# Performance work log

Measured on AMD Instinct MI355X. Metric: run time of the kernel, lower is better.

Reference implementation:

```python
import jax, jax.numpy as jnp
import numpy as np

N_NODES = 100000
N_EDGES = 1600000
D_IN = 128
D_HID = 128
SCALE = 1.8
EPS = 1e-12


def setup_inputs() -> dict:
    key = jax.random.key(0)
    ks = jax.random.split(key, 7)
    x = jax.random.normal(ks[0], (N_NODES, D_IN), dtype=jnp.float32)
    W1 = jax.random.normal(ks[1], (D_HID, D_IN), dtype=jnp.float32) * 0.05
    b1 = jax.random.normal(ks[2], (D_HID,), dtype=jnp.float32) * 0.05
    W2 = jax.random.normal(ks[3], (D_HID, D_HID), dtype=jnp.float32) * 0.05
    b2 = jax.random.normal(ks[4], (D_HID,), dtype=jnp.float32) * 0.05
    src = jax.random.randint(ks[5], (N_EDGES,), 0, N_NODES, dtype=jnp.int64 if jax.config.jax_enable_x64 else jnp.int32)
    dst = jax.random.randint(ks[6], (N_EDGES,), 0, N_NODES, dtype=jnp.int64 if jax.config.jax_enable_x64 else jnp.int32)
    return {"x": x, "W1": W1, "b1": b1, "W2": W2, "b2": b2, "src": src, "dst": dst}


def reference(x, W1, b1, W2, b2, src, dst):
    N = x.shape[0]
    ones = jnp.ones((src.shape[0],), dtype=x.dtype)
    # GraphConv norm='both' degree normalizers (clamped to >=1 as in DGL)
    deg_out = jnp.maximum(jnp.zeros((N,), x.dtype).at[src].add(ones), 1.0)
    deg_in = jnp.maximum(jnp.zeros((N,), x.dtype).at[dst].add(ones), 1.0)
    norm_out = jax.lax.rsqrt(deg_out)[:, None]  # [N,1]
    norm_in = jax.lax.rsqrt(deg_in)[:, None]    # [N,1]

    def layer(h, W, b):
        # torch.nn.Linear: h @ W.T + b
        h = jnp.einsum('nd,kd->nk', h, W) + b
        # F.normalize(h, dim=1) * 1.8
        nrm = jnp.sqrt(jnp.sum(h * h, axis=1, keepdims=True))
        h = h / jnp.maximum(nrm, EPS) * SCALE
        # GraphConv (weight=False, bias=False, norm='both'):
        # D_out^{-1/2} -> sparse aggregate -> D_in^{-1/2}
        h = h * norm_out
        agg = jax.ops.segment_sum(h[src], dst, num_segments=N)
        return agg * norm_in

    h = layer(x, W1, b1)
    h = layer(h, W2, b2)
    return h
```

## Files before the change

kernel.cpp:

```cpp
#include <hip/hip_runtime.h>
#include <cstdint>
#include <cstddef>

#define D 128
#define NSCALE 1.8f
#define NEPS 1e-12f
#define EPB 2048
#define NBPAD 784
#define NLO 512
#define SCAP 9216
#define SRCB 23
#define SRCM 0x7FFFFF

typedef __attribute__((ext_vector_type(8))) short bf16x8;
typedef __attribute__((ext_vector_type(4))) float f32x4;

__device__ __forceinline__ ushort bf16_rtn(float f) {
    uint32_t u = __float_as_uint(f);
    u = u + 0x7FFFu + ((u >> 16) & 1u);
    return (ushort)(u >> 16);
}

__device__ __forceinline__ float blo(uint32_t u) { return __uint_as_float(u << 16); }
__device__ __forceinline__ float bhi(uint32_t u) { return __uint_as_float(u & 0xFFFF0000u); }

__global__ __launch_bounds__(256) void hist_high_kernel(const int* __restrict__ src,
                                                        const int* __restrict__ dst,
                                                        int* __restrict__ Hd,
                                                        int* __restrict__ Hs, int ne) {
    __shared__ int hd[256], hs[256];
    int t = threadIdx.x, b = blockIdx.x;
    hd[t] = 0; hs[t] = 0;
    __syncthreads();
    int base = b * EPB, end = min(ne, base + EPB);
    for (int i = base + t; i < end; i += 256) {
        atomicAdd(&hd[dst[i] >> 9], 1);
        atomicAdd(&hs[src[i] >> 9], 1);
    }
    __syncthreads();
    Hd[t * NBPAD + b] = hd[t];
    Hs[t * NBPAD + b] = hs[t];
}

__global__ __launch_bounds__(256) void scan_cols_kernel(int* __restrict__ Hd,
                                                        int* __restrict__ Hs,
                                                        int* __restrict__ total_d,
                                                        int* __restrict__ total_s, int nbk) {
    __shared__ int s[256];
    int* H = blockIdx.y ? Hs : Hd;
    int* tot = blockIdx.y ? total_s : total_d;
    int v = blockIdx.x, t = threadIdx.x;
    int base = v * NBPAD + 4 * t;
    int a0 = (4 * t + 0 < nbk) ? H[base + 0] : 0;
    int a1 = (4 * t + 1 < nbk) ? H[base + 1] : 0;
    int a2 = (4 * t + 2 < nbk) ? H[base + 2] : 0;
    int a3 = (4 * t + 3 < nbk) ? H[base + 3] : 0;
    int sum = a0 + a1 + a2 + a3;
    s[t] = sum;
    __syncthreads();
    #pragma unroll
    for (int off = 1; off < 256; off <<= 1) {
        int u = (t >= off) ? s[t - off] : 0;
        __syncthreads();
        s[t] += u;
        __syncthreads();
    }
    int excl = s[t] - sum;
    if (4 * t + 0 < nbk) H[base + 0] = excl;
    if (4 * t + 1 < nbk) H[base + 1] = excl + a0;
    if (4 * t + 2 < nbk) H[base + 2] = excl + a0 + a1;
    if (4 * t + 3 < nbk) H[base + 3] = excl + a0 + a1 + a2;
    if (t == 255) tot[v] = s[255];
}

__global__ __launch_bounds__(256) void scan_tot_kernel(const int* __restrict__ total_d,
                                                       const int* __restrict__ total_s,
                                                       int* __restrict__ Bd,
                                                       int* __restrict__ Bs, int hb) {
    __shared__ int s[256];
    const int* tot = blockIdx.x ? total_s : total_d;
    int* B = blockIdx.x ? Bs : Bd;
    int t = threadIdx.x;
    int val = (t < hb) ? tot[t] : 0;
    s[t] = val;
    __syncthreads();
    #pragma unroll
    for (int off = 1; off < 256; off <<= 1) {
        int u = (t >= off) ? s[t - off] : 0;
        __syncthreads();
        s[t] += u;
        __syncthreads();
    }
    if (t <= hb) B[t] = s[t] - val;
}

__global__ __launch_bounds__(256) void scatter_high_kernel(const int* __restrict__ src,
                                                           const int* __restrict__ dst,
                                                           const int* __restrict__ Hd,
                                                           const int* __restrict__ Hs,
                                                           const int* __restrict__ Bd,
                                                           const int* __restrict__ Bs,
                                                           uint32_t* __restrict__ spack,
                                                           ushort* __restrict__ ss_low,
                                                           int ne, int hb) {
    __shared__ int cur_d[256], cur_s[256];
    int t = threadIdx.x, b = blockIdx.x;
    if (t < hb) {
        cur_d[t] = Bd[t] + Hd[t * NBPAD + b];
        cur_s[t] = Bs[t] + Hs[t * NBPAD + b];
    }
    __syncthreads();
    int base = b * EPB, end = min(ne, base + EPB);
    for (int i = base + t; i < end; i += 256) {
        int d = dst[i], s = src[i];
        int pd = atomicAdd(&cur_d[d >> 9], 1);
        spack[pd] = ((uint32_t)(d & (NLO - 1)) << SRCB) | (uint32_t)s;
        int ps = atomicAdd(&cur_s[s >> 9], 1);
        ss_low[ps] = (ushort)(s & (NLO - 1));
    }
}

__global__ __launch_bounds__(1024) void bucket_sort_kernel(const uint32_t* __restrict__ spack,
                                                           const int* __restrict__ Bd,
                                                           int* __restrict__ offs,
                                                           int* __restrict__ cnt_dst,
                                                           float* __restrict__ norm_in,
                                                           int* __restrict__ ssrc, int N) {
    __shared__ int h[NLO], sc[NLO], cur[NLO];
    __shared__ int stage[SCAP];
    int t = threadIdx.x, v = blockIdx.x;
    int beg = Bd[v], end = Bd[v + 1];
    int m = end - beg;
    if (t < NLO) h[t] = 0;
    __syncthreads();
    for (int i = beg + t; i < end; i += 1024) atomicAdd(&h[spack[i] >> SRCB], 1);
    __syncthreads();
    int cnt = 0;
    if (t < NLO) { cnt = h[t]; sc[t] = cnt; }
    __syncthreads();
    #pragma unroll
    for (int off = 1; off < NLO; off <<= 1) {
        int u = (t >= off && t < NLO) ? sc[t - off] : 0;
        __syncthreads();
        if (t < NLO) sc[t] += u;
        __syncthreads();
    }
    int excl = (t < NLO) ? (sc[t] - cnt) : 0;
    int g = (v << 9) + t;
    if (t < NLO && g < N) {
        offs[g] = beg + excl;
        cnt_dst[g] = cnt;
        norm_in[g] = rsqrtf((float)max(cnt, 1));
    }
    if (m <= SCAP) {
        if (t < NLO) cur[t] = excl;
        __syncthreads();
        for (int i = beg + t; i < end; i += 1024) {
            uint32_t p = spack[i];
            int pos = atomicAdd(&cur[p >> SRCB], 1);
            stage[pos] = (int)(p & SRCM);
        }
        __syncthreads();
        for (int j = t; j < m; j += 1024) ssrc[beg + j] = stage[j];
    } else {
        if (t < NLO) cur[t] = beg + excl;
        __syncthreads();
        for (int i = beg + t; i < end; i += 1024) {
            uint32_t p = spack[i];
            int pos = atomicAdd(&cur[p >> SRCB], 1);
            ssrc[pos] = (int)(p & SRCM);
        }
    }
}

__global__ __launch_bounds__(1024) void bucket_hist_kernel(const ushort* __restrict__ ss_low,
                                                           const int* __restrict__ Bs,
                                                           float* __restrict__ norm_out, int N) {
    __shared__ int h[NLO];
    int t = threadIdx.x, v = blockIdx.x;
    int beg = Bs[v], end = Bs[v + 1];
    if (t < NLO) h[t] = 0;
    __syncthreads();
    for (int i = beg + t; i < end; i += 1024) atomicAdd(&h[(int)ss_low[i]], 1);
    __syncthreads();
    int g = (v << 9) + t;
    if (t < NLO && g < N) norm_out[g] = rsqrtf((float)max(h[t], 1));
}

__global__ __launch_bounds__(256) void mlp_mfma_kernel(const float* __restrict__ X,
                                                       const float* __restrict__ W,
                                                       const float* __restrict__ b,
                                                       const float* __restrict__ post,
                                                       ushort* __restrict__ Abuf, int N) {
    __shared__ ushort Wf[128 * 128];

    const int t = threadIdx.x;
    const int wave = t >> 6;
    const int lane = t & 63;
    const int q = lane >> 4;
    const int l16 = lane & 15;

    if (blockIdx.x == 0 && t < 16) {
        ((uint4*)(Abuf + (size_t)N * D))[t] = make_uint4(0u, 0u, 0u, 0u);
    }

    #pragma unroll
    for (int it = 0; it < 8; ++it) {
        int f = t + 256 * it;
        int j = f >> 8;
        int p = (f >> 6) & 3;
        int ln = f & 63;
        int n = 16 * j + (ln & 15);
        int k0 = 32 * p + 8 * (ln >> 4);
        const float* srcp = W + n * D + k0;
        float4 a0 = *(const float4*)(srcp);
        float4 a1 = *(const float4*)(srcp + 4);
        bf16x8 v;
        v[0] = (short)bf16_rtn(a0.x); v[1] = (short)bf16_rtn(a0.y);
        v[2] = (short)bf16_rtn(a0.z); v[3] = (short)bf16_rtn(a0.w);
        v[4] = (short)bf16_rtn(a1.x); v[5] = (short)bf16_rtn(a1.y);
        v[6] = (short)bf16_rtn(a1.z); v[7] = (short)bf16_rtn(a1.w);
        ((bf16x8*)Wf)[f] = v;
    }

    const int r0 = blockIdx.x * 128 + wave * 32;
    bf16x8 ahi[2][4], alo[2][4];
    #pragma unroll
    for (int rt = 0; rt < 2; ++rt) {
        int row = r0 + rt * 16 + l16;
        bool ok = (row < N);
        const float* xr = X + (size_t)(ok ? row : 0) * D;
        #pragma unroll
        for (int p = 0; p < 4; ++p) {
            int k0 = 32 * p + 8 * q;
            float4 a0 = ok ? *(const float4*)(xr + k0)     : make_float4(0, 0, 0, 0);
            float4 a1 = ok ? *(const float4*)(xr + k0 + 4) : make_float4(0, 0, 0, 0);
            float fv[8] = {a0.x, a0.y, a0.z, a0.w, a1.x, a1.y, a1.z, a1.w};
            bf16x8 h, l;
            #pragma unroll
            for (int e = 0; e < 8; ++e) {
                uint32_t u = __float_as_uint(fv[e]);
                h[e] = (short)(u >> 16);
                float hf = __uint_as_float(u & 0xFFFF0000u);
                l[e] = (short)(__float_as_uint(fv[e] - hf) >> 16);
            }
            ahi[rt][p] = h;
            alo[rt][p] = l;
        }
    }

    __syncthreads();

    f32x4 acc[2][8];
    #pragma unroll
    for (int rt = 0; rt < 2; ++rt)
        #pragma unroll
        for (int j = 0; j < 8; ++j) acc[rt][j] = (f32x4){0.f, 0.f, 0.f, 0.f};

    #pragma unroll
    for (int j = 0; j < 8; ++j) {
        #pragma unroll
        for (int p = 0; p < 4; ++p) {
            bf16x8 bb = ((bf16x8*)Wf)[(j * 4 + p) * 64 + lane];
            acc[0][j] = __builtin_amdgcn_mfma_f32_16x16x32_bf16(ahi[0][p], bb, acc[0][j], 0, 0, 0);
            acc[0][j] = __builtin_amdgcn_mfma_f32_16x16x32_bf16(alo[0][p], bb, acc[0][j], 0, 0, 0);
            acc[1][j] = __builtin_amdgcn_mfma_f32_16x16x32_bf16(ahi[1][p], bb, acc[1][j], 0, 0, 0);
            acc[1][j] = __builtin_amdgcn_mfma_f32_16x16x32_bf16(alo[1][p], bb, acc[1][j], 0, 0, 0);
        }
    }

    float bias[8];
    #pragma unroll
    for (int j = 0; j < 8; ++j) bias[j] = b[16 * j + l16];

    #pragma unroll
    for (int rt = 0; rt < 2; ++rt) {
        float ss[4] = {0.f, 0.f, 0.f, 0.f};
        #pragma unroll
        for (int j = 0; j < 8; ++j)
            #pragma unroll
            for (int r = 0; r < 4; ++r) {
                float v = acc[rt][j][r] + bias[j];
                acc[rt][j][r] = v;
                ss[r] += v * v;
            }
        #pragma unroll
        for (int m = 1; m <= 8; m <<= 1)
            #pragma unroll
            for (int r = 0; r < 4; ++r) ss[r] += __shfl_xor(ss[r], m);

        #pragma unroll
        for (int r = 0; r < 4; ++r) {
            int row = r0 + rt * 16 + 4 * q + r;
            if (row < N) {
                float f = NSCALE / fmaxf(sqrtf(ss[r]), NEPS) * post[row];
                #pragma unroll
                for (int j = 0; j < 8; ++j)
                    Abuf[(size_t)row * D + 16 * j + l16] = bf16_rtn(acc[rt][j][r] * f);
            }
        }
    }
}

__global__ __launch_bounds__(256) void agg_kernel(const ushort* __restrict__ A,
                                                  const int* __restrict__ sorted_src,
                                                  const int* __restrict__ offs,
                                                  const int* __restrict__ cnt,
                                                  const float* __restrict__ norm_in,
                                                  float* __restrict__ out, int N) {
    int wave = threadIdx.x >> 6;
    int n0 = (blockIdx.x * 4 + wave) * 2;
    if (n0 >= N) return;
    int lane = threadIdx.x & 63;
    int g = lane >> 4;
    int c = lane & 15;
    const ushort* Ac = A + c * 8;

    int n1 = n0 + 1;
    int beg0 = offs[n0], len0 = cnt[n0];
    int beg1 = 0, len1 = 0;
    if (n1 < N) { beg1 = offs[n1]; len1 = cnt[n1]; }
    int last0 = beg0 + len0 - 1;
    int last1 = beg1 + len1 - 1;

    float a0[8] = {0.f, 0.f, 0.f, 0.f, 0.f, 0.f, 0.f, 0.f};
    float a1[8] = {0.f, 0.f, 0.f, 0.f, 0.f, 0.f, 0.f, 0.f};

    int mx = max(len0, len1);
    for (int i = 0; i < mx; i += 16) {
        int idx[8];
        #pragma unroll
        for (int k = 0; k < 4; ++k) {
            int e = beg0 + i + g + 4 * k;
            int cl = max(min(e, last0), 0);
            idx[k] = sorted_src[cl];
            if (e > last0) idx[k] = N;
        }
        #pragma unroll
        for (int k = 0; k < 4; ++k) {
            int e = beg1 + i + g + 4 * k;
            int cl = max(min(e, last1), 0);
            idx[4 + k] = sorted_src[cl];
            if (e > last1) idx[4 + k] = N;
        }
        uint4 w[8];
        #pragma unroll
        for (int k = 0; k < 8; ++k) w[k] = *(const uint4*)(Ac + (size_t)idx[k] * D);
        #pragma unroll
        for (int k = 0; k < 4; ++k) {
            a0[0] += blo(w[k].x); a0[1] += bhi(w[k].x);
            a0[2] += blo(w[k].y); a0[3] += bhi(w[k].y);
            a0[4] += blo(w[k].z); a0[5] += bhi(w[k].z);
            a0[6] += blo(w[k].w); a0[7] += bhi(w[k].w);
        }
        #pragma unroll
        for (int k = 4; k < 8; ++k) {
            a1[0] += blo(w[k].x); a1[1] += bhi(w[k].x);
            a1[2] += blo(w[k].y); a1[3] += bhi(w[k].y);
            a1[4] += blo(w[k].z); a1[5] += bhi(w[k].z);
            a1[6] += blo(w[k].w); a1[7] += bhi(w[k].w);
        }
    }

    #pragma unroll
    for (int e = 0; e < 8; ++e) {
        a0[e] += __shfl_xor(a0[e], 16);
        a0[e] += __shfl_xor(a0[e], 32);
        a1[e] += __shfl_xor(a1[e], 16);
        a1[e] += __shfl_xor(a1[e], 32);
    }

    if (g == 0) {
        float sc0 = norm_in[n0];
        float* op0 = out + (size_t)n0 * D + c * 8;
        *(float4*)(op0)     = make_float4(a0[0] * sc0, a0[1] * sc0, a0[2] * sc0, a0[3] * sc0);
        *(float4*)(op0 + 4) = make_float4(a0[4] * sc0, a0[5] * sc0, a0[6] * sc0, a0[7] * sc0);
        if (n1 < N) {
            float sc1 = norm_in[n1];
            float* op1 = out + (size_t)n1 * D + c * 8;
            *(float4*)(op1)     = make_float4(a1[0] * sc1, a1[1] * sc1, a1[2] * sc1, a1[3] * sc1);
            *(float4*)(op1 + 4) = make_float4(a1[4] * sc1, a1[5] * sc1, a1[6] * sc1, a1[7] * sc1);
        }
    }
}


extern "C" void kernel_launch(void* const* d_in, const int* in_sizes, int n_in,
                              void* d_out, int out_size, void* d_ws, size_t ws_size,
                              hipStream_t stream) {
    const float* x  = (const float*)d_in[0];
    const float* W1 = (const float*)d_in[1];
    const float* b1 = (const float*)d_in[2];
    const float* W2 = (const float*)d_in[3];
    const float* b2 = (const float*)d_in[4];
    const int* src  = (const int*)d_in[5];
    const int* dst  = (const int*)d_in[6];
    float* out = (float*)d_out;

    const int N  = in_sizes[0] / D;
    const int NE = in_sizes[5];
    const int NBK = (NE + EPB - 1) / EPB;
    const int HB  = (N + NLO - 1) / NLO;

    char* w = (char*)d_ws;
    auto take = [&](size_t bytes) { char* p = w; w += (bytes + 255) & ~(size_t)255; return p; };
    int*      Hd       = (int*)take((size_t)256 * NBPAD * 4);
    int*      Hs       = (int*)take((size_t)256 * NBPAD * 4);
    int*      total_d  = (int*)take(256 * 4);
    int*      total_s  = (int*)take(256 * 4);
    int*      Bd       = (int*)take((size_t)(HB + 1) * 4);
    int*      Bs       = (int*)take((size_t)(HB + 1) * 4);
    uint32_t* spack    = (uint32_t*)take((size_t)NE * 4);
    ushort*   ss_low   = (ushort*)take((size_t)NE * 2);
    int*      ssrc     = (int*)take((size_t)NE * 4);
    int*      offs     = (int*)take((size_t)N * 4);
    int*      cnt_dst  = (int*)take((size_t)N * 4);
    float*    norm_in  = (float*)take((size_t)N * 4);
    float*    norm_out = (float*)take((size_t)N * 4);
    ushort*   Abuf     = (ushort*)take((size_t)(N + 1) * D * 2);

    hist_high_kernel<<<NBK, 256, 0, stream>>>(src, dst, Hd, Hs, NE);
    scan_cols_kernel<<<dim3(HB, 2), 256, 0, stream>>>(Hd, Hs, total_d, total_s, NBK);
    scan_tot_kernel<<<2, 256, 0, stream>>>(total_d, total_s, Bd, Bs, HB);
    scatter_high_kernel<<<NBK, 256, 0, stream>>>(src, dst, Hd, Hs, Bd, Bs,
                                                 spack, ss_low, NE, HB);
    bucket_sort_kernel<<<HB, 1024, 0, stream>>>(spack, Bd, offs, cnt_dst, norm_in, ssrc, N);
    bucket_hist_kernel<<<HB, 1024, 0, stream>>>(ss_low, Bs, norm_out, N);

    const int mlp_blocks = (N + 127) / 128;
    const int agg_blocks = (N + 7) / 8;

    mlp_mfma_kernel<<<mlp_blocks, 256, 0, stream>>>(x, W1, b1, norm_out, Abuf, N);
    agg_kernel<<<agg_blocks, 256, 0, stream>>>(Abuf, ssrc, offs, cnt_dst, norm_in, out, N);

    mlp_mfma_kernel<<<mlp_blocks, 256, 0, stream>>>(out, W2, b2, norm_out, Abuf, N);
    agg_kernel<<<agg_blocks, 256, 0, stream>>>(Abuf, ssrc, offs, cnt_dst, norm_in, out, N);
}
```

Measured before the change: 333.2 us.

## Apply W2 before aggregation using linearity and fuse both MLPs into one kernel

```diff
diff --git a/kernel.cpp b/kernel.cpp
--- a/kernel.cpp
+++ b/kernel.cpp
@@ -120,15 +120,30 @@
     }
 }
 
-__global__ __launch_bounds__(1024) void bucket_sort_kernel(const uint32_t* __restrict__ spack,
-                                                           const int* __restrict__ Bd,
-                                                           int* __restrict__ offs,
-                                                           int* __restrict__ cnt_dst,
-                                                           float* __restrict__ norm_in,
-                                                           int* __restrict__ ssrc, int N) {
+__global__ __launch_bounds__(1024) void bucket_sorthist_kernel(const uint32_t* __restrict__ spack,
+                                                               const int* __restrict__ Bd,
+                                                               const ushort* __restrict__ ss_low,
+                                                               const int* __restrict__ Bs,
+                                                               int* __restrict__ offs,
+                                                               int* __restrict__ cnt_dst,
+                                                               float* __restrict__ norm_in,
+                                                               float* __restrict__ norm_out,
+                                                               int* __restrict__ ssrc, int N) {
     __shared__ int h[NLO], sc[NLO], cur[NLO];
     __shared__ int stage[SCAP];
     int t = threadIdx.x, v = blockIdx.x;
+
+    if (blockIdx.y == 1) {
+        int beg = Bs[v], end = Bs[v + 1];
+        if (t < NLO) h[t] = 0;
+        __syncthreads();
+        for (int i = beg + t; i < end; i += 1024) atomicAdd(&h[(int)ss_low[i]], 1);
+        __syncthreads();
+        int g = (v << 9) + t;
+        if (t < NLO && g < N) norm_out[g] = rsqrtf((float)max(h[t], 1));
+        return;
+    }
+
     int beg = Bd[v], end = Bd[v + 1];
     int m = end - beg;
     if (t < NLO) h[t] = 0;
@@ -173,25 +188,13 @@
     }
 }
 
-__global__ __launch_bounds__(1024) void bucket_hist_kernel(const ushort* __restrict__ ss_low,
-                                                           const int* __restrict__ Bs,
-                                                           float* __restrict__ norm_out, int N) {
-    __shared__ int h[NLO];
-    int t = threadIdx.x, v = blockIdx.x;
-    int beg = Bs[v], end = Bs[v + 1];
-    if (t < NLO) h[t] = 0;
-    __syncthreads();
-    for (int i = beg + t; i < end; i += 1024) atomicAdd(&h[(int)ss_low[i]], 1);
-    __syncthreads();
-    int g = (v << 9) + t;
-    if (t < NLO && g < N) norm_out[g] = rsqrtf((float)max(h[t], 1));
-}
-
-__global__ __launch_bounds__(256) void mlp_mfma_kernel(const float* __restrict__ X,
-                                                       const float* __restrict__ W,
-                                                       const float* __restrict__ b,
-                                                       const float* __restrict__ post,
-                                                       ushort* __restrict__ Abuf, int N) {
+__global__ __launch_bounds__(256) void mlp_fused_kernel(const float* __restrict__ X,
+                                                        const float* __restrict__ W1,
+                                                        const float* __restrict__ b1,
+                                                        const float* __restrict__ W2,
+                                                        const float* __restrict__ post,
+                                                        ushort* __restrict__ Q,
+                                                        ushort* __restrict__ Abuf, int N) {
     __shared__ ushort Wf[128 * 128];
 
     const int t = threadIdx.x;
@@ -200,8 +203,9 @@
     const int q = lane >> 4;
     const int l16 = lane & 15;
 
-    if (blockIdx.x == 0 && t < 16) {
-        ((uint4*)(Abuf + (size_t)N * D))[t] = make_uint4(0u, 0u, 0u, 0u);
+    if (blockIdx.x == 0 && t < 32) {
+        if (t < 16) ((uint4*)(Q    + (size_t)N * D))[t]      = make_uint4(0u, 0u, 0u, 0u);
+        else        ((uint4*)(Abuf + (size_t)N * D))[t - 16] = make_uint4(0u, 0u, 0u, 0u);
     }
 
     #pragma unroll
@@ -210,9 +214,10 @@
         int j = f >> 8;
         int p = (f >> 6) & 3;
         int ln = f & 63;
-        int n = 16 * j + (ln & 15);
+        int m = ln & 15;
+        int row = 32 * (j >> 1) + 8 * (m >> 2) + 4 * (j & 1) + (m & 3);
         int k0 = 32 * p + 8 * (ln >> 4);
-        const float* srcp = W + n * D + k0;
+        const float* srcp = W1 + row * D + k0;
         float4 a0 = *(const float4*)(srcp);
         float4 a1 = *(const float4*)(srcp + 4);
         bf16x8 v;
@@ -224,7 +229,7 @@
     }
 
     const int r0 = blockIdx.x * 128 + wave * 32;
-    bf16x8 ahi[2][4], alo[2][4];
+    bf16x8 xhi[2][4], xlo[2][4];
     #pragma unroll
     for (int rt = 0; rt < 2; ++rt) {
         int row = r0 + rt * 16 + l16;
@@ -244,60 +249,242 @@
                 float hf = __uint_as_float(u & 0xFFFF0000u);
                 l[e] = (short)(__float_as_uint(fv[e] - hf) >> 16);
             }
-            ahi[rt][p] = h;
-            alo[rt][p] = l;
-        }
-    }
-
-    __syncthreads();
-
-    f32x4 acc[2][8];
+            xhi[rt][p] = h;
+            xlo[rt][p] = l;
+        }
+    }
+
+    __syncthreads();
+
+    f32x4 acc1[2][8];
     #pragma unroll
     for (int rt = 0; rt < 2; ++rt)
         #pragma unroll
-        for (int j = 0; j < 8; ++j) acc[rt][j] = (f32x4){0.f, 0.f, 0.f, 0.f};
+        for (int j = 0; j < 8; ++j) acc1[rt][j] = (f32x4){0.f, 0.f, 0.f, 0.f};
 
     #pragma unroll
     for (int j = 0; j < 8; ++j) {
         #pragma unroll
         for (int p = 0; p < 4; ++p) {
-            bf16x8 bb = ((bf16x8*)Wf)[(j * 4 + p) * 64 + lane];
-            acc[0][j] = __builtin_amdgcn_mfma_f32_16x16x32_bf16(ahi[0][p], bb, acc[0][j], 0, 0, 0);
-            acc[0][j] = __builtin_amdgcn_mfma_f32_16x16x32_bf16(alo[0][p], bb, acc[0][j], 0, 0, 0);
-            acc[1][j] = __builtin_amdgcn_mfma_f32_16x16x32_bf16(ahi[1][p], bb, acc[1][j], 0, 0, 0);
-            acc[1][j] = __builtin_amdgcn_mfma_f32_16x16x32_bf16(alo[1][p], bb, acc[1][j], 0, 0, 0);
-        }
-    }
-
-    float bias[8];
-    #pragma unroll
-    for (int j = 0; j < 8; ++j) bias[j] = b[16 * j + l16];
+            bf16x8 wf = ((bf16x8*)Wf)[(j * 4 + p) * 64 + lane];
+            acc1[0][j] = __builtin_amdgcn_mfma_f32_16x16x32_bf16(wf, xhi[0][p], acc1[0][j], 0, 0, 0);
+            acc1[0][j] = __builtin_amdgcn_mfma_f32_16x16x32_bf16(wf, xlo[0][p], acc1[0][j], 0, 0, 0);
+            acc1[1][j] = __builtin_amdgcn_mfma_f32_16x16x32_bf16(wf, xhi[1][p], acc1[1][j], 0, 0, 0);
+            acc1[1][j] = __builtin_amdgcn_mfma_f32_16x16x32_bf16(wf, xlo[1][p], acc1[1][j], 0, 0, 0);
+        }
+    }
 
     #pragma unroll
     for (int rt = 0; rt < 2; ++rt) {
-        float ss[4] = {0.f, 0.f, 0.f, 0.f};
-        #pragma unroll
-        for (int j = 0; j < 8; ++j)
+        int node = r0 + rt * 16 + l16;
+        float po = (node < N) ? post[node] : 0.f;
+        float ss = 0.f;
+        #pragma unroll
+        for (int j = 0; j < 8; ++j) {
+            const float4 bq = *(const float4*)(b1 + 32 * (j >> 1) + 8 * q + 4 * (j & 1));
+            float v0 = acc1[rt][j][0] + bq.x; acc1[rt][j][0] = v0; ss += v0 * v0;
+            float v1 = acc1[rt][j][1] + bq.y; acc1[rt][j][1] = v1; ss += v1 * v1;
+            float v2 = acc1[rt][j][2] + bq.z; acc1[rt][j][2] = v2; ss += v2 * v2;
+            float v3 = acc1[rt][j][3] + bq.w; acc1[rt][j][3] = v3; ss += v3 * v3;
+        }
+        ss += __shfl_xor(ss, 16);
+        ss += __shfl_xor(ss, 32);
+        float fsc = NSCALE / fmaxf(sqrtf(ss), NEPS) * po;
+        #pragma unroll
+        for (int j = 0; j < 8; ++j) {
+            acc1[rt][j][0] *= fsc; acc1[rt][j][1] *= fsc;
+            acc1[rt][j][2] *= fsc; acc1[rt][j][3] *= fsc;
+        }
+    }
+
+    bf16x8 p2h[2][4], p2l[2][4];
+    #pragma unroll
+    for (int rt = 0; rt < 2; ++rt) {
+        #pragma unroll
+        for (int p = 0; p < 4; ++p) {
+            bf16x8 hh, ll;
             #pragma unroll
-            for (int r = 0; r < 4; ++r) {
-                float v = acc[rt][j][r] + bias[j];
-                acc[rt][j][r] = v;
-                ss[r] += v * v;
+            for (int e = 0; e < 8; ++e) {
+                float vv = acc1[rt][2 * p + (e >> 2)][e & 3];
+                uint32_t u = __float_as_uint(vv);
+                hh[e] = (short)(u >> 16);
+                float hf = __uint_as_float(u & 0xFFFF0000u);
+                ll[e] = (short)(__float_as_uint(vv - hf) >> 16);
             }
-        #pragma unroll
-        for (int m = 1; m <= 8; m <<= 1)
+            p2h[rt][p] = hh;
+            p2l[rt][p] = ll;
+        }
+    }
+
+    __syncthreads();
+    #pragma unroll
+    for (int it = 0; it < 8; ++it) {
+        int f = t + 256 * it;
+        int j = f >> 8;
+        int p = (f >> 6) & 3;
+        int ln = f & 63;
+        int row = 16 * j + (ln & 15);
+        int k0 = 32 * p + 8 * (ln >> 4);
+        const float* srcp = W2 + row * D + k0;
+        float4 a0 = *(const float4*)(srcp);
+        float4 a1 = *(const float4*)(srcp + 4);
+        bf16x8 v;
+        v[0] = (short)bf16_rtn(a0.x); v[1] = (short)bf16_rtn(a0.y);
+        v[2] = (short)bf16_rtn(a0.z); v[3] = (short)bf16_rtn(a0.w);
+        v[4] = (short)bf16_rtn(a1.x); v[5] = (short)bf16_rtn(a1.y);
+        v[6] = (short)bf16_rtn(a1.z); v[7] = (short)bf16_rtn(a1.w);
+        ((bf16x8*)Wf)[f] = v;
+    }
+    __syncthreads();
+
+    f32x4 acc2[2][8];
+    #pragma unroll
+    for (int rt = 0; rt < 2; ++rt)
+        #pragma unroll
+        for (int j = 0; j < 8; ++j) acc2[rt][j] = (f32x4){0.f, 0.f, 0.f, 0.f};
+
+    #pragma unroll
+    for (int j = 0; j < 8; ++j) {
+        #pragma unroll
+        for (int p = 0; p < 4; ++p) {
+            bf16x8 wf = ((bf16x8*)Wf)[(j * 4 + p) * 64 + lane];
+            acc2[0][j] = __builtin_amdgcn_mfma_f32_16x16x32_bf16(wf, p2h[0][p], acc2[0][j], 0, 0, 0);
+            acc2[0][j] = __builtin_amdgcn_mfma_f32_16x16x32_bf16(wf, p2l[0][p], acc2[0][j], 0, 0, 0);
+            acc2[1][j] = __builtin_amdgcn_mfma_f32_16x16x32_bf16(wf, p2h[1][p], acc2[1][j], 0, 0, 0);
+            acc2[1][j] = __builtin_amdgcn_mfma_f32_16x16x32_bf16(wf, p2l[1][p], acc2[1][j], 0, 0, 0);
+        }
+    }
+
+    #pragma unroll
+    for (int rt = 0; rt < 2; ++rt) {
+        int node = r0 + rt * 16 + l16;
+        if (node < N) {
+            ushort* qp = Q + (size_t)node * D + 4 * q;
             #pragma unroll
-            for (int r = 0; r < 4; ++r) ss[r] += __shfl_xor(ss[r], m);
-
-        #pragma unroll
-        for (int r = 0; r < 4; ++r) {
-            int row = r0 + rt * 16 + 4 * q + r;
-            if (row < N) {
-                float f = NSCALE / fmaxf(sqrtf(ss[r]), NEPS) * post[row];
-                #pragma unroll
-                for (int j = 0; j < 8; ++j)
-                    Abuf[(size_t)row * D + 16 * j + l16] = bf16_rtn(acc[rt][j][r] * f);
+            for (int j = 0; j < 8; ++j) {
+                ushort4 s4;
+                s4.x = bf16_rtn(acc2[rt][j][0]);
+                s4.y = bf16_rtn(acc2[rt][j][1]);
+                s4.z = bf16_rtn(acc2[rt][j][2]);
+                s4.w = bf16_rtn(acc2[rt][j][3]);
+                *(ushort4*)(qp + 16 * j) = s4;
             }
+        }
+    }
+}
+
+__global__ __launch_bounds__(256) void agg_mid_kernel(const ushort* __restrict__ A,
+                                                      const int* __restrict__ sorted_src,
+                                                      const int* __restrict__ offs,
+                                                      const int* __restrict__ cnt,
+                                                      const float* __restrict__ norm_in,
+                                                      const float* __restrict__ norm_out,
+                                                      const float* __restrict__ b2,
+                                                      ushort* __restrict__ Abuf, int N) {
+    int wave = threadIdx.x >> 6;
+    int n0 = (blockIdx.x * 4 + wave) * 2;
+    if (n0 >= N) return;
+    int lane = threadIdx.x & 63;
+    int g = lane >> 4;
+    int c = lane & 15;
+    const ushort* Ac = A + c * 8;
+
+    int n1 = n0 + 1;
+    int beg0 = offs[n0], len0 = cnt[n0];
+    int beg1 = 0, len1 = 0;
+    if (n1 < N) { beg1 = offs[n1]; len1 = cnt[n1]; }
+    int last0 = beg0 + len0 - 1;
+    int last1 = beg1 + len1 - 1;
+
+    float a0[8] = {0.f, 0.f, 0.f, 0.f, 0.f, 0.f, 0.f, 0.f};
+    float a1[8] = {0.f, 0.f, 0.f, 0.f, 0.f, 0.f, 0.f, 0.f};
+
+    int mx = max(len0, len1);
+    for (int i = 0; i < mx; i += 16) {
+        int idx[8];
+        #pragma unroll
+        for (int k = 0; k < 4; ++k) {
+            int e = beg0 + i + g + 4 * k;
+            int cl = max(min(e, last0), 0);
+            idx[k] = sorted_src[cl];
+            if (e > last0) idx[k] = N;
+        }
+        #pragma unroll
+        for (int k = 0; k < 4; ++k) {
+            int e = beg1 + i + g + 4 * k;
+            int cl = max(min(e, last1), 0);
+            idx[4 + k] = sorted_src[cl];
+            if (e > last1) idx[4 + k] = N;
+        }
+        uint4 w[8];
+        #pragma unroll
+        for (int k = 0; k < 8; ++k) w[k] = *(const uint4*)(Ac + (size_t)idx[k] * D);
+        #pragma unroll
+        for (int k = 0; k < 4; ++k) {
+            a0[0] += blo(w[k].x); a0[1] += bhi(w[k].x);
+            a0[2] += blo(w[k].y); a0[3] += bhi(w[k].y);
+            a0[4] += blo(w[k].z); a0[5] += bhi(w[k].z);
+            a0[6] += blo(w[k].w); a0[7] += bhi(w[k].w);
+        }
+        #pragma unroll
+        for (int k = 4; k < 8; ++k) {
+            a1[0] += blo(w[k].x); a1[1] += bhi(w[k].x);
+            a1[2] += blo(w[k].y); a1[3] += bhi(w[k].y);
+            a1[4] += blo(w[k].z); a1[5] += bhi(w[k].z);
+            a1[6] += blo(w[k].w); a1[7] += bhi(w[k].w);
+        }
+    }
+
+    #pragma unroll
+    for (int e = 0; e < 8; ++e) {
+        a0[e] += __shfl_xor(a0[e], 16);
+        a0[e] += __shfl_xor(a0[e], 32);
+        a1[e] += __shfl_xor(a1[e], 16);
+        a1[e] += __shfl_xor(a1[e], 32);
+    }
+
+    float4 bql = *(const float4*)(b2 + c * 8);
+    float4 bqh = *(const float4*)(b2 + c * 8 + 4);
+    float bb[8] = {bql.x, bql.y, bql.z, bql.w, bqh.x, bqh.y, bqh.z, bqh.w};
+
+    {
+        float ni = norm_in[n0];
+        float y[8];
+        float ss = 0.f;
+        #pragma unroll
+        for (int e = 0; e < 8; ++e) { y[e] = a0[e] * ni + bb[e]; ss += y[e] * y[e]; }
+        ss += __shfl_xor(ss, 1); ss += __shfl_xor(ss, 2);
+        ss += __shfl_xor(ss, 4); ss += __shfl_xor(ss, 8);
+        float fsc = NSCALE / fmaxf(sqrtf(ss), NEPS) * norm_out[n0];
+        if (g == 0) {
+            ushort4 s0, s1;
+            s0.x = bf16_rtn(y[0] * fsc); s0.y = bf16_rtn(y[1] * fsc);
+            s0.z = bf16_rtn(y[2] * fsc); s0.w = bf16_rtn(y[3] * fsc);
+            s1.x = bf16_rtn(y[4] * fsc); s1.y = bf16_rtn(y[5] * fsc);
+            s1.z = bf16_rtn(y[6] * fsc); s1.w = bf16_rtn(y[7] * fsc);
+            ushort* op = Abuf + (size_t)n0 * D + c * 8;
+            *(ushort4*)(op) = s0;
+            *(ushort4*)(op + 4) = s1;
+        }
+    }
+    if (n1 < N) {
+        float ni = norm_in[n1];
+        float y[8];
+        float ss = 0.f;
+        #pragma unroll
+        for (int e = 0; e < 8; ++e) { y[e] = a1[e] * ni + bb[e]; ss += y[e] * y[e]; }
+        ss += __shfl_xor(ss, 1); ss += __shfl_xor(ss, 2);
+        ss += __shfl_xor(ss, 4); ss += __shfl_xor(ss, 8);
+        float fsc = NSCALE / fmaxf(sqrtf(ss), NEPS) * norm_out[n1];
+        if (g == 0) {
+            ushort4 s0, s1;
+            s0.x = bf16_rtn(y[0] * fsc); s0.y = bf16_rtn(y[1] * fsc);
+            s0.z = bf16_rtn(y[2] * fsc); s0.w = bf16_rtn(y[3] * fsc);
+            s1.x = bf16_rtn(y[4] * fsc); s1.y = bf16_rtn(y[5] * fsc);
+            s1.z = bf16_rtn(y[6] * fsc); s1.w = bf16_rtn(y[7] * fsc);
+            ushort* op = Abuf + (size_t)n1 * D + c * 8;
+            *(ushort4*)(op) = s0;
+            *(ushort4*)(op + 4) = s1;
         }
     }
 }
@@ -417,6 +604,7 @@
     int*      cnt_dst  = (int*)take((size_t)N * 4);
     float*    norm_in  = (float*)take((size_t)N * 4);
     float*    norm_out = (float*)take((size_t)N * 4);
+    ushort*   Qbuf     = (ushort*)take((size_t)(N + 1) * D * 2);
     ushort*   Abuf     = (ushort*)take((size_t)(N + 1) * D * 2);
 
     hist_high_kernel<<<NBK, 256, 0, stream>>>(src, dst, Hd, Hs, NE);
@@ -424,15 +612,15 @@
     scan_tot_kernel<<<2, 256, 0, stream>>>(total_d, total_s, Bd, Bs, HB);
     scatter_high_kernel<<<NBK, 256, 0, stream>>>(src, dst, Hd, Hs, Bd, Bs,
                                                  spack, ss_low, NE, HB);
-    bucket_sort_kernel<<<HB, 1024, 0, stream>>>(spack, Bd, offs, cnt_dst, norm_in, ssrc, N);
-    bucket_hist_kernel<<<HB, 1024, 0, stream>>>(ss_low, Bs, norm_out, N);
+    bucket_sorthist_kernel<<<dim3(HB, 2), 1024, 0, stream>>>(spack, Bd, ss_low, Bs,
+                                                             offs, cnt_dst, norm_in,
+                                                             norm_out, ssrc, N);
 
     const int mlp_blocks = (N + 127) / 128;
     const int agg_blocks = (N + 7) / 8;
 
-    mlp_mfma_kernel<<<mlp_blocks, 256, 0, stream>>>(x, W1, b1, norm_out, Abuf, N);
+    mlp_fused_kernel<<<mlp_blocks, 256, 0, stream>>>(x, W1, b1, W2, norm_out, Qbuf, Abuf, N);
+    agg_mid_kernel<<<agg_blocks, 256, 0, stream>>>(Qbuf, ssrc, offs, cnt_dst,
+                                                   norm_in, norm_out, b2, Abuf, N);
     agg_kernel<<<agg_blocks, 256, 0, stream>>>(Abuf, ssrc, offs, cnt_dst, norm_in, out, N);
-
-    mlp_mfma_kernel<<<mlp_blocks, 256, 0, stream>>>(out, W2, b2, norm_out, Abuf, N);
-    agg_kernel<<<agg_blocks, 256, 0, stream>>>(Abuf, ssrc, offs, cnt_dst, norm_in, out, N);
-}
+}
```

Result: faster. 323.5 us (-2.9%).
